# Kernel optimization log

Measured on AMD Instinct MI355X. Metric: run time of the kernel, lower is better.

## Reference

```python
import jax, jax.numpy as jnp
import numpy as np

WINDOW_SIZE = 11
SIGMA = 1.5
C1 = 0.01 ** 2
C2 = 0.03 ** 2


def _make_window(window_size, channel):
    x = np.arange(window_size) - window_size // 2
    g = np.exp(-(x ** 2) / (2.0 * SIGMA ** 2))
    g = g / g.sum()
    w2d = np.outer(g, g).astype(np.float32)  # [K,K]
    # depthwise kernel [C, 1, K, K]
    return jnp.asarray(np.broadcast_to(w2d, (channel, 1, window_size, window_size)).copy())


def _dw_conv(x, window, channel):
    pad = WINDOW_SIZE // 2
    return jax.lax.conv_general_dilated(
        x, window, window_strides=(1, 1), padding=[(pad, pad), (pad, pad)],
        dimension_numbers=('NCHW', 'OIHW', 'NCHW'), feature_group_count=channel)


def setup_inputs() -> dict:
    key = jax.random.key(0)
    k1, k2 = jax.random.split(key)
    shape = (16, 3, 512, 512)
    img1 = jax.random.uniform(k1, shape, dtype=jnp.float32)
    img2 = jax.random.uniform(k2, shape, dtype=jnp.float32)
    return {"img1": img1, "img2": img2}


def reference(img1, img2):
    channel = img1.shape[1]
    window = _make_window(WINDOW_SIZE, channel).astype(img1.dtype)

    mu1 = _dw_conv(img1, window, channel)
    mu2 = _dw_conv(img2, window, channel)
    mu1_sq = mu1 * mu1
    mu2_sq = mu2 * mu2
    mu1_mu2 = mu1 * mu2

    sigma1_sq = _dw_conv(img1 * img1, window, channel) - mu1_sq
    sigma2_sq = _dw_conv(img2 * img2, window, channel) - mu2_sq
    sigma12 = _dw_conv(img1 * img2, window, channel) - mu1_mu2

    ssim_map = ((2 * mu1_mu2 + C1) * (2 * sigma12 + C2)) / (
        (mu1_sq + mu2_sq + C1) * (sigma1_sq + sigma2_sq + C2))
    return jnp.mean(ssim_map)  # size_average=True
```

## Files before the change

kernel.cpp:

```cpp
#include <hip/hip_runtime.h>
#include <math.h>

#define IMG_H 512
#define IMG_W 512
#define TH 4
#define KR 5
#define KS 11
#define NR (TH + 2 * KR)
#define LW2 524
#define NTHREADS 512
#define NBANDS (IMG_H / TH)
#define NPLANES 48
#define NBLK (NBANDS * NPLANES)

typedef float f32x2 __attribute__((ext_vector_type(2)));

struct W22 { float w[2 * KS]; };

__device__ __forceinline__ int swz(int u) { return u ^ ((u >> 3) & 7); }

__global__ __launch_bounds__(NTHREADS)
void ssim_tile_kernel(const float* __restrict__ img1, const float* __restrict__ img2,
                      float* __restrict__ bsums, W22 wt) {
    __shared__ __align__(16) f32x2 sm[TH][LW2];
    __shared__ __align__(16) f32x2 sv[TH][LW2];
    __shared__ float redw[NTHREADS / 64];

    const int bid   = blockIdx.x;
    const int sbid  = (bid & 7) * (NBLK / 8) + (bid >> 3);
    const int plane = sbid >> 7;
    const int band  = sbid & (NBANDS - 1);

    const int row0 = band * TH;
    const float* __restrict__ p1 = img1 + (size_t)plane * (IMG_H * IMG_W);
    const float* __restrict__ p2 = img2 + (size_t)plane * (IMG_H * IMG_W);
    const int tid = threadIdx.x;
    const int r0  = row0 - KR;

    if (tid < 12) {
        const int e = (tid < 6) ? tid : (512 + tid);
        const int slot = swz(e >> 1) * 2 + (e & 1);
        #pragma unroll
        for (int r = 0; r < TH; ++r) {
            sm[r][slot] = (f32x2){0.f, 0.f};
            sv[r][slot] = (f32x2){0.f, 0.f};
        }
    }

    float av[NR], bv[NR];
    {
        const float* __restrict__ g1 = p1 + tid;
        const float* __restrict__ g2 = p2 + tid;
        if (r0 >= 0 && r0 + NR <= IMG_H) {
            #pragma unroll
            for (int j = 0; j < NR; ++j) {
                av[j] = g1[(r0 + j) * IMG_W];
                bv[j] = g2[(r0 + j) * IMG_W];
            }
        } else {
            #pragma unroll
            for (int j = 0; j < NR; ++j) {
                const int  rr  = r0 + j;
                const bool ok  = (rr >= 0) && (rr < IMG_H);
                const int  rrc = min(max(rr, 0), IMG_H - 1);
                const float a = g1[rrc * IMG_W];
                const float b = g2[rrc * IMG_W];
                av[j] = ok ? a : 0.f;
                bv[j] = ok ? b : 0.f;
            }
        }
    }

    f32x2 accm[TH], accs[TH];
    #pragma unroll
    for (int r = 0; r < TH; ++r) { accm[r] = (f32x2){0.f, 0.f}; accs[r] = (f32x2){0.f, 0.f}; }

    #pragma unroll
    for (int j = 0; j < NR; ++j) {
        const float a = av[j], b = bv[j];
        f32x2 mv; mv.x = a;                mv.y = b;
        f32x2 pv; pv.x = fmaf(a, a, b*b);  pv.y = a * b;
        #pragma unroll
        for (int r = 0; r < TH; ++r) {
            const int k = j - r;
            if (k >= 0 && k < KS) {
                f32x2 wv; wv.x = wt.w[2*k]; wv.y = wt.w[2*k + 1];
                accm[r] = __builtin_elementwise_fma(wv, mv, accm[r]);
                accs[r] = __builtin_elementwise_fma(wv, pv, accs[r]);
            }
        }
    }
    {
        const int e = tid + 6;
        const int slot = swz(e >> 1) * 2 + (e & 1);
        #pragma unroll
        for (int r = 0; r < TH; ++r) {
            sm[r][slot] = accm[r];
            sv[r][slot] = accs[r];
        }
    }
    __syncthreads();

    const float C1f = 0.0001f;
    const float C2f = 0.0009f;
    const int r  = tid >> 7;
    const int L  = tid & 127;
    const int u0 = L << 1;

    int su[8];
    #pragma unroll
    for (int i = 0; i < 8; ++i) su[i] = swz(u0 + i);

    f32x2 cmu[4], csv[4];
    {
        f32x2 xm[16];
        const float4* rpm = (const float4*)&sm[r][0];
        #pragma unroll
        for (int i = 0; i < 8; ++i) {
            const float4 q = rpm[su[i]];
            xm[2*i]   = (f32x2){q.x, q.y};
            xm[2*i+1] = (f32x2){q.z, q.w};
        }
        #pragma unroll
        for (int j = 0; j < 4; ++j) {
            f32x2 w0; w0.x = wt.w[0]; w0.y = wt.w[1];
            f32x2 m = w0 * xm[j + 1];
            #pragma unroll
            for (int k = 1; k < KS; ++k) {
                f32x2 wv; wv.x = wt.w[2*k]; wv.y = wt.w[2*k + 1];
                m = __builtin_elementwise_fma(wv, xm[j + 1 + k], m);
            }
            cmu[j] = m;
        }
    }
    {
        f32x2 xs[16];
        const float4* rps = (const float4*)&sv[r][0];
        #pragma unroll
        for (int i = 0; i < 8; ++i) {
            const float4 q = rps[su[i]];
            xs[2*i]   = (f32x2){q.x, q.y};
            xs[2*i+1] = (f32x2){q.z, q.w};
        }
        #pragma unroll
        for (int j = 0; j < 4; ++j) {
            f32x2 w0; w0.x = wt.w[0]; w0.y = wt.w[1];
            f32x2 m = w0 * xs[j + 1];
            #pragma unroll
            for (int k = 1; k < KS; ++k) {
                f32x2 wv; wv.x = wt.w[2*k]; wv.y = wt.w[2*k + 1];
                m = __builtin_elementwise_fma(wv, xs[j + 1 + k], m);
            }
            csv[j] = m;
        }
    }

    float lsum = 0.f;
    #pragma unroll
    for (int j = 0; j < 4; ++j) {
        const float m1 = cmu[j].x, m2 = cmu[j].y;
        const float mu11 = m1 * m1;
        const float mu22 = m2 * m2;
        const float mu12 = m1 * m2;
        const float t     = mu11 + mu22;
        const float sigpp = csv[j].x - t;
        const float sig12 = csv[j].y - mu12;
        const float num = fmaf(2.f, mu12, C1f) * fmaf(2.f, sig12, C2f);
        const float den = (t + C1f) * (sigpp + C2f);
        lsum = fmaf(num, __builtin_amdgcn_rcpf(den), lsum);
    }

    #pragma unroll
    for (int off = 32; off > 0; off >>= 1) lsum += __shfl_down(lsum, off);
    if ((tid & 63) == 0) redw[tid >> 6] = lsum;
    __syncthreads();
    if (tid == 0) {
        float t = 0.f;
        #pragma unroll
        for (int w = 0; w < NTHREADS / 64; ++w) t += redw[w];
        bsums[sbid] = t;
    }
}

__global__ __launch_bounds__(256)
void ssim_reduce_kernel(const float4* __restrict__ bsums, int n4,
                        float* __restrict__ out, double inv_count) {
    __shared__ double red[256];
    double acc = 0.0;
    for (int i = threadIdx.x; i < n4; i += 256) {
        const float4 v = bsums[i];
        acc += (double)v.x + (double)v.y + (double)v.z + (double)v.w;
    }
    red[threadIdx.x] = acc;
    __syncthreads();
    #pragma unroll
    for (int off = 128; off > 0; off >>= 1) {
        if (threadIdx.x < off) red[threadIdx.x] += red[threadIdx.x + off];
        __syncthreads();
    }
    if (threadIdx.x == 0) out[0] = (float)(red[0] * inv_count);
}

extern "C" void kernel_launch(void* const* d_in, const int* in_sizes, int n_in,
                              void* d_out, int out_size, void* d_ws, size_t ws_size,
                              hipStream_t stream) {
    const float* img1 = (const float*)d_in[0];
    const float* img2 = (const float*)d_in[1];
    float* out = (float*)d_out;
    float* bsums = (float*)d_ws;

    W22 wt;
    {
        double g[KS], sum = 0.0;
        for (int i = 0; i < KS; ++i) {
            const double x = (double)(i - KR);
            g[i] = exp(-(x * x) / (2.0 * 1.5 * 1.5));
            sum += g[i];
        }
        for (int i = 0; i < KS; ++i) {
            wt.w[2*i]     = (float)(g[i] / sum);
            wt.w[2*i + 1] = (float)(g[i] / sum);
        }
    }

    ssim_tile_kernel<<<dim3(NBLK), NTHREADS, 0, stream>>>(img1, img2, bsums, wt);

    const double inv_count = 1.0 / ((double)NPLANES * IMG_H * IMG_W);
    ssim_reduce_kernel<<<1, 256, 0, stream>>>((const float4*)bsums, NBLK / 4,
                                              out, inv_count);
}
```

Baseline: 44.08 us.

## Split rows into half-width column tiles with interleaved float4 shared layout

After: 60.91 us. 1.38x slower.

```diff
diff --git a/kernel.cpp b/kernel.cpp
--- a/kernel.cpp
+++ b/kernel.cpp
@@ -3,55 +3,54 @@
 
 #define IMG_H 512
 #define IMG_W 512
+#define TW 256
 #define TH 4
 #define KR 5
 #define KS 11
 #define NR (TH + 2 * KR)
-#define LW2 524
-#define NTHREADS 512
+#define NSTRIP (TW + 2 * KR)
+#define LWE 268
+#define NTHREADS 256
+#define NXT (IMG_W / TW)
 #define NBANDS (IMG_H / TH)
 #define NPLANES 48
-#define NBLK (NBANDS * NPLANES)
+#define NBLK (NXT * NBANDS * NPLANES)
 
 typedef float f32x2 __attribute__((ext_vector_type(2)));
+typedef float f32x4 __attribute__((ext_vector_type(4)));
 
 struct W22 { float w[2 * KS]; };
 
-__device__ __forceinline__ int swz(int u) { return u ^ ((u >> 3) & 7); }
-
-__global__ __launch_bounds__(NTHREADS)
+__device__ __forceinline__ int swz(int e) { return e ^ ((e >> 3) & 7); }
+
+__global__ __launch_bounds__(NTHREADS, 8)
 void ssim_tile_kernel(const float* __restrict__ img1, const float* __restrict__ img2,
                       float* __restrict__ bsums, W22 wt) {
-    __shared__ __align__(16) f32x2 sm[TH][LW2];
-    __shared__ __align__(16) f32x2 sv[TH][LW2];
+    __shared__ f32x4 sE[TH][LWE];
     __shared__ float redw[NTHREADS / 64];
 
     const int bid   = blockIdx.x;
     const int sbid  = (bid & 7) * (NBLK / 8) + (bid >> 3);
-    const int plane = sbid >> 7;
-    const int band  = sbid & (NBANDS - 1);
-
-    const int row0 = band * TH;
+    const int xt    = sbid & 1;
+    const int band  = (sbid >> 1) & (NBANDS - 1);
+    const int plane = sbid >> 8;
+
+    const int C0 = xt * TW;
+    const int r0 = band * TH - KR;
     const float* __restrict__ p1 = img1 + (size_t)plane * (IMG_H * IMG_W);
     const float* __restrict__ p2 = img2 + (size_t)plane * (IMG_H * IMG_W);
     const int tid = threadIdx.x;
-    const int r0  = row0 - KR;
-
-    if (tid < 12) {
-        const int e = (tid < 6) ? tid : (512 + tid);
-        const int slot = swz(e >> 1) * 2 + (e & 1);
-        #pragma unroll
-        for (int r = 0; r < TH; ++r) {
-            sm[r][slot] = (f32x2){0.f, 0.f};
-            sv[r][slot] = (f32x2){0.f, 0.f};
-        }
-    }
-
-    float av[NR], bv[NR];
-    {
-        const float* __restrict__ g1 = p1 + tid;
-        const float* __restrict__ g2 = p2 + tid;
-        if (r0 >= 0 && r0 + NR <= IMG_H) {
+    const bool yint = (r0 >= 0) && (r0 + NR <= IMG_H);
+
+    for (int s = tid; s < NSTRIP; s += NTHREADS) {
+        const int   col  = C0 - KR + s;
+        const int   colc = min(max(col, 0), IMG_W - 1);
+        const float sel  = (col >= 0 && col < IMG_W) ? 1.f : 0.f;
+        const float* __restrict__ g1 = p1 + colc;
+        const float* __restrict__ g2 = p2 + colc;
+
+        float av[NR], bv[NR];
+        if (yint) {
             #pragma unroll
             for (int j = 0; j < NR; ++j) {
                 av[j] = g1[(r0 + j) * IMG_W];
@@ -69,102 +68,99 @@
                 bv[j] = ok ? b : 0.f;
             }
         }
-    }
-
-    f32x2 accm[TH], accs[TH];
-    #pragma unroll
-    for (int r = 0; r < TH; ++r) { accm[r] = (f32x2){0.f, 0.f}; accs[r] = (f32x2){0.f, 0.f}; }
-
-    #pragma unroll
-    for (int j = 0; j < NR; ++j) {
-        const float a = av[j], b = bv[j];
-        f32x2 mv; mv.x = a;                mv.y = b;
-        f32x2 pv; pv.x = fmaf(a, a, b*b);  pv.y = a * b;
+        asm volatile("" :: "v"(av[0]), "v"(av[1]), "v"(av[2]), "v"(av[3]),
+                           "v"(av[4]), "v"(av[5]), "v"(av[6]), "v"(av[7]),
+                           "v"(av[8]), "v"(av[9]), "v"(av[10]), "v"(av[11]),
+                           "v"(av[12]), "v"(av[13]));
+        asm volatile("" :: "v"(bv[0]), "v"(bv[1]), "v"(bv[2]), "v"(bv[3]),
+                           "v"(bv[4]), "v"(bv[5]), "v"(bv[6]), "v"(bv[7]),
+                           "v"(bv[8]), "v"(bv[9]), "v"(bv[10]), "v"(bv[11]),
+                           "v"(bv[12]), "v"(bv[13]));
+
+        f32x2 accm[TH], accs[TH];
+        #pragma unroll
+        for (int r = 0; r < TH; ++r) { accm[r] = (f32x2){0.f, 0.f}; accs[r] = (f32x2){0.f, 0.f}; }
+
+        #pragma unroll
+        for (int j = 0; j < NR; ++j) {
+            const float a = av[j], b = bv[j];
+            f32x2 mv; mv.x = a;                 mv.y = b;
+            f32x2 pv; pv.x = fmaf(a, a, b * b); pv.y = a * b;
+            #pragma unroll
+            for (int r = 0; r < TH; ++r) {
+                const int k = j - r;
+                if (k >= 0 && k < KS) {
+                    f32x2 wv; wv.x = wt.w[2*k]; wv.y = wt.w[2*k + 1];
+                    accm[r] = __builtin_elementwise_fma(wv, mv, accm[r]);
+                    accs[r] = __builtin_elementwise_fma(wv, pv, accs[r]);
+                }
+            }
+        }
+
+        const f32x2 sel2 = {sel, sel};
+        const int slot = swz(s);
         #pragma unroll
         for (int r = 0; r < TH; ++r) {
-            const int k = j - r;
-            if (k >= 0 && k < KS) {
-                f32x2 wv; wv.x = wt.w[2*k]; wv.y = wt.w[2*k + 1];
-                accm[r] = __builtin_elementwise_fma(wv, mv, accm[r]);
-                accs[r] = __builtin_elementwise_fma(wv, pv, accs[r]);
-            }
-        }
-    }
-    {
-        const int e = tid + 6;
-        const int slot = swz(e >> 1) * 2 + (e & 1);
-        #pragma unroll
-        for (int r = 0; r < TH; ++r) {
-            sm[r][slot] = accm[r];
-            sv[r][slot] = accs[r];
+            const f32x2 m = accm[r] * sel2;
+            const f32x2 v = accs[r] * sel2;
+            sE[r][slot] = (f32x4){m.x, m.y, v.x, v.y};
         }
     }
     __syncthreads();
 
     const float C1f = 0.0001f;
     const float C2f = 0.0009f;
-    const int r  = tid >> 7;
-    const int L  = tid & 127;
-    const int u0 = L << 1;
-
-    int su[8];
-    #pragma unroll
-    for (int i = 0; i < 8; ++i) su[i] = swz(u0 + i);
-
-    f32x2 cmu[4], csv[4];
+    const int r  = tid >> 6;
+    const int L  = tid & 63;
+    const int e0 = L << 2;
+    f32x4 acc[4];
+    #pragma unroll
+    for (int jj = 0; jj < 4; ++jj) acc[jj] = (f32x4){0.f, 0.f, 0.f, 0.f};
+
     {
-        f32x2 xm[16];
-        const float4* rpm = (const float4*)&sm[r][0];
-        #pragma unroll
-        for (int i = 0; i < 8; ++i) {
-            const float4 q = rpm[su[i]];
-            xm[2*i]   = (f32x2){q.x, q.y};
-            xm[2*i+1] = (f32x2){q.z, q.w};
-        }
-        #pragma unroll
-        for (int j = 0; j < 4; ++j) {
-            f32x2 w0; w0.x = wt.w[0]; w0.y = wt.w[1];
-            f32x2 m = w0 * xm[j + 1];
-            #pragma unroll
-            for (int k = 1; k < KS; ++k) {
-                f32x2 wv; wv.x = wt.w[2*k]; wv.y = wt.w[2*k + 1];
-                m = __builtin_elementwise_fma(wv, xm[j + 1 + k], m);
-            }
-            cmu[j] = m;
+        f32x4 x[8];
+        #pragma unroll
+        for (int i = 0; i < 8; ++i) x[i] = sE[r][swz(e0 + i)];
+        #pragma unroll
+        for (int jj = 0; jj < 4; ++jj) {
+            #pragma unroll
+            for (int k = 0; k < KS; ++k) {
+                if (jj + k < 8) {
+                    f32x4 wv; wv.x = wt.w[2*k]; wv.y = wt.w[2*k+1];
+                    wv.z = wt.w[2*k]; wv.w = wt.w[2*k+1];
+                    acc[jj] = __builtin_elementwise_fma(wv, x[jj + k], acc[jj]);
+                }
+            }
         }
     }
     {
-        f32x2 xs[16];
-        const float4* rps = (const float4*)&sv[r][0];
-        #pragma unroll
-        for (int i = 0; i < 8; ++i) {
-            const float4 q = rps[su[i]];
-            xs[2*i]   = (f32x2){q.x, q.y};
-            xs[2*i+1] = (f32x2){q.z, q.w};
-        }
-        #pragma unroll
-        for (int j = 0; j < 4; ++j) {
-            f32x2 w0; w0.x = wt.w[0]; w0.y = wt.w[1];
-            f32x2 m = w0 * xs[j + 1];
-            #pragma unroll
-            for (int k = 1; k < KS; ++k) {
-                f32x2 wv; wv.x = wt.w[2*k]; wv.y = wt.w[2*k + 1];
-                m = __builtin_elementwise_fma(wv, xs[j + 1 + k], m);
-            }
-            csv[j] = m;
+        f32x4 x[6];
+        #pragma unroll
+        for (int i = 0; i < 6; ++i) x[i] = sE[r][swz(e0 + 8 + i)];
+        #pragma unroll
+        for (int jj = 0; jj < 4; ++jj) {
+            #pragma unroll
+            for (int k = 0; k < KS; ++k) {
+                if (jj + k >= 8) {
+                    f32x4 wv; wv.x = wt.w[2*k]; wv.y = wt.w[2*k+1];
+                    wv.z = wt.w[2*k]; wv.w = wt.w[2*k+1];
+                    acc[jj] = __builtin_elementwise_fma(wv, x[jj + k - 8], acc[jj]);
+                }
+            }
         }
     }
 
     float lsum = 0.f;
     #pragma unroll
-    for (int j = 0; j < 4; ++j) {
-        const float m1 = cmu[j].x, m2 = cmu[j].y;
+    for (int jj = 0; jj < 4; ++jj) {
+        const float m1 = acc[jj].x, m2 = acc[jj].y;
+        const float pp = acc[jj].z, ab = acc[jj].w;
         const float mu11 = m1 * m1;
         const float mu22 = m2 * m2;
         const float mu12 = m1 * m2;
         const float t     = mu11 + mu22;
-        const float sigpp = csv[j].x - t;
-        const float sig12 = csv[j].y - mu12;
+        const float sigpp = pp - t;
+        const float sig12 = ab - mu12;
         const float num = fmaf(2.f, mu12, C1f) * fmaf(2.f, sig12, C2f);
         const float den = (t + C1f) * (sigpp + C2f);
         lsum = fmaf(num, __builtin_amdgcn_rcpf(den), lsum);
```

## Process two row bands per block with double-buffered LDS to overlap loads

Applied to the files above, without the earlier changes.

Result: slower. 47.32 us (+7.4%).

```diff
diff --git a/kernel.cpp b/kernel.cpp
--- a/kernel.cpp
+++ b/kernel.cpp
@@ -9,9 +9,9 @@
 #define NR (TH + 2 * KR)
 #define LW2 524
 #define NTHREADS 512
-#define NBANDS (IMG_H / TH)
+#define NPAIRS 64
 #define NPLANES 48
-#define NBLK (NBANDS * NPLANES)
+#define NBLK (NPAIRS * NPLANES)
 
 typedef float f32x2 __attribute__((ext_vector_type(2)));
 
@@ -19,67 +19,42 @@
 
 __device__ __forceinline__ int swz(int u) { return u ^ ((u >> 3) & 7); }
 
-__global__ __launch_bounds__(NTHREADS)
-void ssim_tile_kernel(const float* __restrict__ img1, const float* __restrict__ img2,
-                      float* __restrict__ bsums, W22 wt) {
-    __shared__ __align__(16) f32x2 sm[TH][LW2];
-    __shared__ __align__(16) f32x2 sv[TH][LW2];
-    __shared__ float redw[NTHREADS / 64];
-
-    const int bid   = blockIdx.x;
-    const int sbid  = (bid & 7) * (NBLK / 8) + (bid >> 3);
-    const int plane = sbid >> 7;
-    const int band  = sbid & (NBANDS - 1);
-
-    const int row0 = band * TH;
-    const float* __restrict__ p1 = img1 + (size_t)plane * (IMG_H * IMG_W);
-    const float* __restrict__ p2 = img2 + (size_t)plane * (IMG_H * IMG_W);
-    const int tid = threadIdx.x;
-    const int r0  = row0 - KR;
-
-    if (tid < 12) {
-        const int e = (tid < 6) ? tid : (512 + tid);
-        const int slot = swz(e >> 1) * 2 + (e & 1);
-        #pragma unroll
-        for (int r = 0; r < TH; ++r) {
-            sm[r][slot] = (f32x2){0.f, 0.f};
-            sv[r][slot] = (f32x2){0.f, 0.f};
-        }
-    }
-
-    float av[NR], bv[NR];
-    {
-        const float* __restrict__ g1 = p1 + tid;
-        const float* __restrict__ g2 = p2 + tid;
-        if (r0 >= 0 && r0 + NR <= IMG_H) {
-            #pragma unroll
-            for (int j = 0; j < NR; ++j) {
-                av[j] = g1[(r0 + j) * IMG_W];
-                bv[j] = g2[(r0 + j) * IMG_W];
-            }
-        } else {
-            #pragma unroll
-            for (int j = 0; j < NR; ++j) {
-                const int  rr  = r0 + j;
-                const bool ok  = (rr >= 0) && (rr < IMG_H);
-                const int  rrc = min(max(rr, 0), IMG_H - 1);
-                const float a = g1[rrc * IMG_W];
-                const float b = g2[rrc * IMG_W];
-                av[j] = ok ? a : 0.f;
-                bv[j] = ok ? b : 0.f;
-            }
-        }
-    }
-
+__device__ __forceinline__ void load_band(const float* __restrict__ g1,
+                                          const float* __restrict__ g2,
+                                          int r0, float av[NR], float bv[NR]) {
+    if (r0 >= 0 && r0 + NR <= IMG_H) {
+        #pragma unroll
+        for (int j = 0; j < NR; ++j) {
+            av[j] = g1[(r0 + j) * IMG_W];
+            bv[j] = g2[(r0 + j) * IMG_W];
+        }
+    } else {
+        #pragma unroll
+        for (int j = 0; j < NR; ++j) {
+            const int  rr  = r0 + j;
+            const bool ok  = (rr >= 0) && (rr < IMG_H);
+            const int  rrc = min(max(rr, 0), IMG_H - 1);
+            const float a = g1[rrc * IMG_W];
+            const float b = g2[rrc * IMG_W];
+            av[j] = ok ? a : 0.f;
+            bv[j] = ok ? b : 0.f;
+        }
+    }
+}
+
+__device__ __forceinline__ void vconv_store(const float av[NR], const float bv[NR],
+                                            const W22& wt,
+                                            f32x2 (* __restrict__ sm)[LW2],
+                                            f32x2 (* __restrict__ sv)[LW2],
+                                            int slot) {
     f32x2 accm[TH], accs[TH];
     #pragma unroll
     for (int r = 0; r < TH; ++r) { accm[r] = (f32x2){0.f, 0.f}; accs[r] = (f32x2){0.f, 0.f}; }
-
     #pragma unroll
     for (int j = 0; j < NR; ++j) {
         const float a = av[j], b = bv[j];
-        f32x2 mv; mv.x = a;                mv.y = b;
-        f32x2 pv; pv.x = fmaf(a, a, b*b);  pv.y = a * b;
+        f32x2 mv; mv.x = a;                 mv.y = b;
+        f32x2 pv; pv.x = fmaf(a, a, b * b); pv.y = a * b;
         #pragma unroll
         for (int r = 0; r < TH; ++r) {
             const int k = j - r;
@@ -90,27 +65,18 @@
             }
         }
     }
-    {
-        const int e = tid + 6;
-        const int slot = swz(e >> 1) * 2 + (e & 1);
-        #pragma unroll
-        for (int r = 0; r < TH; ++r) {
-            sm[r][slot] = accm[r];
-            sv[r][slot] = accs[r];
-        }
-    }
-    __syncthreads();
-
-    const float C1f = 0.0001f;
-    const float C2f = 0.0009f;
-    const int r  = tid >> 7;
-    const int L  = tid & 127;
-    const int u0 = L << 1;
-
-    int su[8];
-    #pragma unroll
-    for (int i = 0; i < 8; ++i) su[i] = swz(u0 + i);
-
+    #pragma unroll
+    for (int r = 0; r < TH; ++r) {
+        sm[r][slot] = accm[r];
+        sv[r][slot] = accs[r];
+    }
+}
+
+__device__ __forceinline__ float phaseB(const f32x2 (* __restrict__ sm)[LW2],
+                                        const f32x2 (* __restrict__ sv)[LW2],
+                                        const W22& wt, int tid, const int su[8]) {
+    const float C1f = 0.0001f, C2f = 0.0009f;
+    const int r = tid >> 7;
     f32x2 cmu[4], csv[4];
     {
         f32x2 xm[16];
@@ -154,7 +120,6 @@
             csv[j] = m;
         }
     }
-
     float lsum = 0.f;
     #pragma unroll
     for (int j = 0; j < 4; ++j) {
@@ -169,6 +134,73 @@
         const float den = (t + C1f) * (sigpp + C2f);
         lsum = fmaf(num, __builtin_amdgcn_rcpf(den), lsum);
     }
+    return lsum;
+}
+
+__global__ __launch_bounds__(NTHREADS, 4)
+void ssim_tile_kernel(const float* __restrict__ img1, const float* __restrict__ img2,
+                      float* __restrict__ bsums, W22 wt) {
+    __shared__ __align__(16) f32x2 sm0[TH][LW2], sv0[TH][LW2];
+    __shared__ __align__(16) f32x2 sm1[TH][LW2], sv1[TH][LW2];
+    __shared__ float redw[NTHREADS / 64];
+
+    const int bid   = blockIdx.x;
+    const int sbid  = (bid & 7) * (NBLK / 8) + (bid >> 3);
+    const int plane = sbid / NPAIRS;
+    const int q     = sbid - plane * NPAIRS;
+
+    const float* __restrict__ p1 = img1 + (size_t)plane * (IMG_H * IMG_W);
+    const float* __restrict__ p2 = img2 + (size_t)plane * (IMG_H * IMG_W);
+    const int tid = threadIdx.x;
+    const int r0a = q * 8 - KR;
+    const int r0b = q * 8 + TH - KR;
+
+    if (tid < 12) {
+        const int e = (tid < 6) ? tid : (512 + tid);
+        const int slot = swz(e >> 1) * 2 + (e & 1);
+        #pragma unroll
+        for (int r = 0; r < TH; ++r) {
+            sm0[r][slot] = (f32x2){0.f, 0.f};
+            sv0[r][slot] = (f32x2){0.f, 0.f};
+            sm1[r][slot] = (f32x2){0.f, 0.f};
+            sv1[r][slot] = (f32x2){0.f, 0.f};
+        }
+    }
+
+    const float* __restrict__ g1 = p1 + tid;
+    const float* __restrict__ g2 = p2 + tid;
+    const int e = tid + 6;
+    const int slot = swz(e >> 1) * 2 + (e & 1);
+
+    float av0[NR], bv0[NR];
+    load_band(g1, g2, r0a, av0, bv0);
+    vconv_store(av0, bv0, wt, sm0, sv0, slot);
+
+    float av1[NR], bv1[NR];
+    load_band(g1, g2, r0b, av1, bv1);
+    asm volatile("" :: "v"(av1[0]), "v"(av1[1]), "v"(av1[2]), "v"(av1[3]),
+                       "v"(av1[4]), "v"(av1[5]), "v"(av1[6]), "v"(av1[7]),
+                       "v"(av1[8]), "v"(av1[9]), "v"(av1[10]), "v"(av1[11]),
+                       "v"(av1[12]), "v"(av1[13]));
+    asm volatile("" :: "v"(bv1[0]), "v"(bv1[1]), "v"(bv1[2]), "v"(bv1[3]),
+                       "v"(bv1[4]), "v"(bv1[5]), "v"(bv1[6]), "v"(bv1[7]),
+                       "v"(bv1[8]), "v"(bv1[9]), "v"(bv1[10]), "v"(bv1[11]),
+                       "v"(bv1[12]), "v"(bv1[13]));
+
+    __syncthreads();
+
+    const int L  = tid & 127;
+    const int u0 = L << 1;
+    int su[8];
+    #pragma unroll
+    for (int i = 0; i < 8; ++i) su[i] = swz(u0 + i);
+
+    float lsum = phaseB(sm0, sv0, wt, tid, su);
+
+    vconv_store(av1, bv1, wt, sm1, sv1, slot);
+    __syncthreads();
+
+    lsum += phaseB(sm1, sv1, wt, tid, su);
 
     #pragma unroll
     for (int off = 32; off > 0; off >>= 1) lsum += __shfl_down(lsum, off);
```
